# Kernel optimization log

Hardware: AMD Instinct MI355X
Metric: run time of the kernel (lower is better)

The kernel has to match this reference:

```python
import jax, jax.numpy as jnp
import numpy as np

B, L, LTXT = 4, 1024, 128
D_MODEL, TEXT_DIM = 768, 768
D_INNER, D_STATE, D_CONV, DT_RANK = 2 * D_MODEL, 16, 4, (D_MODEL + 15) // 16


def setup_inputs() -> dict:
    key = jax.random.key(0)
    ks = jax.random.split(key, 10)
    s = 0.02
    f32 = jnp.float32
    # A_log init as in mamba_ssm: A = repeat(arange(1, d_state+1))
    A_log = jnp.log(jnp.broadcast_to(jnp.arange(1, D_STATE + 1, dtype=f32), (D_INNER, D_STATE)))
    return {
        "image_tokens": jax.random.normal(ks[0], (B, L, D_MODEL), f32),
        "text_tokens": jax.random.normal(ks[1], (B, LTXT, TEXT_DIM), f32),
        "W_txt": s * jax.random.normal(ks[2], (D_MODEL, TEXT_DIM), f32),
        "b_txt": jnp.zeros((D_MODEL,), f32),
        "in_proj_w": s * jax.random.normal(ks[3], (2 * D_INNER, D_MODEL), f32),
        "conv_w": s * jax.random.normal(ks[4], (D_INNER, 1, D_CONV), f32),
        "conv_b": jnp.zeros((D_INNER,), f32),
        "x_proj_w": s * jax.random.normal(ks[5], (DT_RANK + 2 * D_STATE, D_INNER), f32),
        "dt_proj_w": s * jax.random.normal(ks[6], (D_INNER, DT_RANK), f32),
        "dt_proj_b": jnp.full((D_INNER,), -4.6, f32),  # inv-softplus of small dt init
        "A_log": A_log,
        "D": jnp.ones((D_INNER,), f32),
        "out_proj_w": s * jax.random.normal(ks[7], (D_MODEL, D_INNER), f32),
    }


def _mamba(tokens, in_proj_w, conv_w, conv_b, x_proj_w, dt_proj_w, dt_proj_b, A_log, D, out_proj_w):
    Bsz = tokens.shape[0]
    # input projection -> x, z each (B, L, d_inner)
    xz = tokens @ in_proj_w.T
    x, z = jnp.split(xz, 2, axis=-1)
    # causal depthwise conv1d over L + SiLU
    x_bdl = jnp.transpose(x, (0, 2, 1))  # (B, d_inner, L)
    x_conv = jax.lax.conv_general_dilated(
        x_bdl, conv_w, (1,), [(D_CONV - 1, 0)],
        dimension_numbers=("NCH", "OIH", "NCH"), feature_group_count=D_INNER,
    ) + conv_b[None, :, None]
    x = jax.nn.silu(jnp.transpose(x_conv, (0, 2, 1)))  # (B, L, d_inner)
    # input-dependent SSM params
    x_dbl = x @ x_proj_w.T  # (B, L, dt_rank + 2*d_state)
    dt_r = x_dbl[..., :DT_RANK]
    Bm = x_dbl[..., DT_RANK:DT_RANK + D_STATE]  # (B, L, d_state)
    Cm = x_dbl[..., DT_RANK + D_STATE:]         # (B, L, d_state)
    dt = jax.nn.softplus(dt_r @ dt_proj_w.T + dt_proj_b)  # (B, L, d_inner)
    A = -jnp.exp(A_log)  # (d_inner, d_state)

    def step(h, inp):
        dt_t, B_t, C_t, u_t = inp  # (B,d_inner),(B,d_state),(B,d_state),(B,d_inner)
        dA = jnp.exp(dt_t[:, :, None] * A)                  # (B, d_inner, d_state)
        h = dA * h + (dt_t * u_t)[:, :, None] * B_t[:, None, :]
        y = jnp.einsum("bds,bs->bd", h, C_t)
        return h, y

    h0 = jnp.zeros((Bsz, D_INNER, D_STATE), tokens.dtype)
    xs = (
        jnp.transpose(dt, (1, 0, 2)),
        jnp.transpose(Bm, (1, 0, 2)),
        jnp.transpose(Cm, (1, 0, 2)),
        jnp.transpose(x, (1, 0, 2)),
    )
    _, ys = jax.lax.scan(step, h0, xs)  # ys: (L, B, d_inner)
    y = jnp.transpose(ys, (1, 0, 2)) + x * D
    y = y * jax.nn.silu(z)
    return y @ out_proj_w.T  # (B, L, d_model)


def reference(image_tokens, text_tokens, W_txt, b_txt, in_proj_w, conv_w, conv_b,
              x_proj_w, dt_proj_w, dt_proj_b, A_log, D, out_proj_w):
    # text_pool='cls' -> take token 0
    txt = text_tokens[:, 0, :] @ W_txt.T + b_txt          # (B, d_model)
    tokens = image_tokens + txt[:, None, :]                # broadcast add
    y = _mamba(tokens, in_proj_w, conv_w, conv_b, x_proj_w,
               dt_proj_w, dt_proj_b, A_log, D, out_proj_w)
    # AdaptiveAvgPool1d(1) over sequence dim, then squeeze -> (B, d_model)
    return y.mean(axis=1)
```

## Files before the change

### kernel.cpp

```cpp
#include <hip/hip_runtime.h>
#include <math.h>

constexpr int kB   = 4;
constexpr int kL   = 1024;
constexpr int kDM  = 768;
constexpr int kDI  = 1536;
constexpr int kDS  = 16;
constexpr int kDTR = 48;
constexpr int kNX  = 80;
constexpr int kM   = kB * kL;
constexpr int kLTXT = 128;

typedef __attribute__((ext_vector_type(8))) short bf16x8;
typedef __attribute__((ext_vector_type(4))) float f32x4;

__device__ inline unsigned short f2bf(float f) {
    unsigned u = __float_as_uint(f);
    u = (u + 0x7FFFu + ((u >> 16) & 1u)) >> 16;
    return (unsigned short)u;
}

__device__ __forceinline__ void gl2lds16(const unsigned short* g, unsigned short* l) {
    __builtin_amdgcn_global_load_lds(
        (const __attribute__((address_space(1))) unsigned int*)g,
        (__attribute__((address_space(3))) unsigned int*)l, 16, 0, 0);
}

__global__ __launch_bounds__(256) void txt_kernel(
    const float* __restrict__ text, const float* __restrict__ Wt,
    const float* __restrict__ bt, float* __restrict__ txt)
{
    int gw = blockIdx.x * 4 + (threadIdx.x >> 6);
    int lane = threadIdx.x & 63;
    int b = gw / kDM;
    int j = gw - b * kDM;
    const float* trow = text + (size_t)b * kLTXT * kDM;
    const float* wrow = Wt + (size_t)j * kDM;
    float acc = 0.f;
    for (int k = lane; k < kDM; k += 64) acc = fmaf(trow[k], wrow[k], acc);
    #pragma unroll
    for (int o = 32; o; o >>= 1) acc += __shfl_xor(acc, o, 64);
    if (lane == 0) txt[gw] = acc + bt[j];
}

__global__ __launch_bounds__(256) void tokens_bf16_kernel(
    const float* __restrict__ img, const float* __restrict__ txt,
    unsigned short* __restrict__ tok)
{
    int i = blockIdx.x * 256 + threadIdx.x;
    float4 a = ((const float4*)img)[i];
    int m = i / (kDM / 4);
    int k4 = i - m * (kDM / 4);
    float4 tv = ((const float4*)(txt + (size_t)(m >> 10) * kDM))[k4];
    ushort4 o;
    o.x = f2bf(a.x + tv.x); o.y = f2bf(a.y + tv.y);
    o.z = f2bf(a.z + tv.z); o.w = f2bf(a.w + tv.w);
    ((ushort4*)tok)[i] = o;
}

__global__ __launch_bounds__(256) void castw_kernel(
    const float* __restrict__ w, unsigned short* __restrict__ o, int n4)
{
    int i = blockIdx.x * 256 + threadIdx.x;
    if (i >= n4) return;
    float4 a = ((const float4*)w)[i];
    ushort4 v;
    v.x = f2bf(a.x); v.y = f2bf(a.y); v.z = f2bf(a.z); v.w = f2bf(a.w);
    ((ushort4*)o)[i] = v;
}

__global__ __launch_bounds__(256) void mfma_inproj_kernel(
    const unsigned short* __restrict__ A, const unsigned short* __restrict__ W,
    float* __restrict__ xout, float* __restrict__ gout)
{
    __shared__ unsigned short Asm[2][128][32];
    __shared__ unsigned short Wsm[2][128][32];
    const int t = threadIdx.x;
    const int lane = t & 63;
    const int wv = t >> 6;
    const int wr = wv >> 1, wc = wv & 1;
    const int m0 = blockIdx.x * 128;
    const int n0 = blockIdx.y * 128;

    const int srow = lane >> 2;
    const int scol = (lane & 3) * 8;
    const unsigned short* agp  = A + (size_t)(m0 + wv * 32 + srow) * kDM + scol;
    const unsigned short* agp2 = agp + 16 * kDM;
    const unsigned short* wgp  = W + (size_t)(n0 + wv * 32 + srow) * kDM + scol;
    const unsigned short* wgp2 = wgp + 16 * kDM;

    auto stage = [&](int buf, int k0) {
        gl2lds16(agp  + k0, &Asm[buf][wv * 32][0]);
        gl2lds16(agp2 + k0, &Asm[buf][wv * 32 + 16][0]);
        gl2lds16(wgp  + k0, &Wsm[buf][wv * 32][0]);
        gl2lds16(wgp2 + k0, &Wsm[buf][wv * 32 + 16][0]);
    };

    f32x4 acc[4][4] = {};
    const int fr = lane & 15;
    const int fk = (lane >> 4) * 8;

    stage(0, 0);
    __syncthreads();

    int buf = 0;
    for (int k0 = 0; k0 < kDM; k0 += 32) {
        if (k0 + 32 < kDM) stage(buf ^ 1, k0 + 32);
        bf16x8 af[4], wf[4];
        #pragma unroll
        for (int i = 0; i < 4; ++i)
            af[i] = *(const bf16x8*)&Asm[buf][wr * 64 + i * 16 + fr][fk];
        #pragma unroll
        for (int j = 0; j < 4; ++j)
            wf[j] = *(const bf16x8*)&Wsm[buf][wc * 64 + j * 16 + fr][fk];
        #pragma unroll
        for (int i = 0; i < 4; ++i)
            #pragma unroll
            for (int j = 0; j < 4; ++j)
                acc[i][j] = __builtin_amdgcn_mfma_f32_16x16x32_bf16(af[i], wf[j], acc[i][j], 0, 0, 0);
        __syncthreads();
        buf ^= 1;
    }

    const int erow = (lane >> 4) * 4;
    const int ecol = lane & 15;
    #pragma unroll
    for (int i = 0; i < 4; ++i) {
        #pragma unroll
        for (int j = 0; j < 4; ++j) {
            const int gn = n0 + wc * 64 + j * 16 + ecol;
            #pragma unroll
            for (int q = 0; q < 4; ++q) {
                const int gm = m0 + wr * 64 + i * 16 + erow + q;
                float v = acc[i][j][q];
                if (gn < kDI) {
                    xout[(size_t)gm * kDI + gn] = v;
                } else {
                    gout[(size_t)gm * kDI + (gn - kDI)] = v / (1.f + __expf(-v));
                }
            }
        }
    }
}

constexpr int kKS   = 8;
constexpr int kKSEG = kDI / kKS;

__global__ __launch_bounds__(256) void xproj_splitk_kernel(
    const float* __restrict__ A, const float* __restrict__ W,
    float* __restrict__ part)
{
    __shared__ float As[16][68];
    __shared__ float Ws[16][84];
    const int t = threadIdx.x;
    const int m0 = blockIdx.x * 64;
    const int kbase = blockIdx.y * kKSEG;
    const int lrow = t >> 2, lk4 = (t & 3) << 2;
    const int ci = (t & 15) << 2;
    const int cj = (t >> 4) * 5;
    float acc[4][5] = {};
    const float* aptr = A + (size_t)(m0 + lrow) * kDI + kbase + lk4;

    for (int k0 = 0; k0 < kKSEG; k0 += 16) {
        float4 av = *(const float4*)(aptr + k0);
        if (k0) __syncthreads();
        As[lk4+0][lrow] = av.x; As[lk4+1][lrow] = av.y;
        As[lk4+2][lrow] = av.z; As[lk4+3][lrow] = av.w;
        #pragma unroll
        for (int i = 0; i < 5; ++i) {
            int idx = t + 256 * i;
            int n = idx % 80;
            int k = idx / 80;
            Ws[k][n] = W[(size_t)n * kDI + kbase + k0 + k];
        }
        __syncthreads();
        #pragma unroll
        for (int k = 0; k < 16; ++k) {
            const float4 a4 = *(const float4*)&As[k][ci];
            const float aa[4] = {a4.x, a4.y, a4.z, a4.w};
            float ww[5];
            #pragma unroll
            for (int j = 0; j < 5; ++j) ww[j] = Ws[k][cj + j];
            #pragma unroll
            for (int i = 0; i < 4; ++i)
                #pragma unroll
                for (int j = 0; j < 5; ++j)
                    acc[i][j] = fmaf(aa[i], ww[j], acc[i][j]);
        }
    }

    float* pbase = part + ((size_t)blockIdx.y * kM) * kNX;
    #pragma unroll
    for (int i = 0; i < 4; ++i)
        #pragma unroll
        for (int j = 0; j < 5; ++j)
            pbase[(size_t)(m0 + ci + i) * kNX + cj + j] = acc[i][j];
}

__global__ __launch_bounds__(256) void xproj_reduce_kernel(
    const float* __restrict__ part, float* __restrict__ xdbl)
{
    int i = blockIdx.x * 256 + threadIdx.x;
    float s = 0.f;
    #pragma unroll
    for (int k = 0; k < kKS; ++k) s += part[(size_t)k * kM * kNX + i];
    xdbl[i] = s;
}

__global__ __launch_bounds__(256) void dtproj_gemm_kernel(
    const float* __restrict__ A, const float* __restrict__ W,
    const float* __restrict__ bias, float* __restrict__ dt)
{
    __shared__ float As[16][68];
    __shared__ float Ws[16][68];
    const int t = threadIdx.x;
    const int m0 = blockIdx.x * 64;
    const int n0 = blockIdx.y * 64;
    const int lrow = t >> 2;
    const int lk4  = (t & 3) << 2;
    const int ci   = (t & 15) << 2;
    const int cj   = (t >> 4) << 2;
    float acc[4][4] = {};
    const float* aptr = A + (size_t)(m0 + lrow) * kNX + lk4;
    const float* wptr = W + (size_t)(n0 + lrow) * kDTR + lk4;

    for (int k0 = 0; k0 < kDTR; k0 += 16) {
        float4 av = *(const float4*)(aptr + k0);
        float4 wv = *(const float4*)(wptr + k0);
        if (k0) __syncthreads();
        As[lk4+0][lrow] = av.x; As[lk4+1][lrow] = av.y;
        As[lk4+2][lrow] = av.z; As[lk4+3][lrow] = av.w;
        Ws[lk4+0][lrow] = wv.x; Ws[lk4+1][lrow] = wv.y;
        Ws[lk4+2][lrow] = wv.z; Ws[lk4+3][lrow] = wv.w;
        __syncthreads();
        #pragma unroll
        for (int k = 0; k < 16; ++k) {
            const float4 a4 = *(const float4*)&As[k][ci];
            const float4 w4 = *(const float4*)&Ws[k][cj];
            const float aa[4] = {a4.x, a4.y, a4.z, a4.w};
            const float ww[4] = {w4.x, w4.y, w4.z, w4.w};
            #pragma unroll
            for (int i = 0; i < 4; ++i)
                #pragma unroll
                for (int j = 0; j < 4; ++j)
                    acc[i][j] = fmaf(aa[i], ww[j], acc[i][j]);
        }
    }

    #pragma unroll
    for (int i = 0; i < 4; ++i) {
        const int gm = m0 + ci + i;
        #pragma unroll
        for (int j = 0; j < 4; ++j) {
            const int gn = n0 + cj + j;
            float v = acc[i][j] + bias[gn];
            v = (v > 20.f) ? v : log1pf(__expf(v));
            dt[(size_t)gm * kDI + gn] = v;
        }
    }
}

__global__ __launch_bounds__(256) void conv_silu_kernel(
    const float* __restrict__ xraw, const float* __restrict__ cw,
    const float* __restrict__ cb, float* __restrict__ xout)
{
    int i = blockIdx.x * 256 + threadIdx.x;
    int d4 = i % (kDI / 4);
    int ml = i / (kDI / 4);
    int l = ml & (kL - 1);
    const int d = d4 * 4;
    float4 acc = *(const float4*)&cb[d];
    const float* base = xraw + (size_t)ml * kDI + d - 3 * (size_t)kDI;
    float4 w0 = *(const float4*)&cw[(d + 0) * 4];
    float4 w1 = *(const float4*)&cw[(d + 1) * 4];
    float4 w2 = *(const float4*)&cw[(d + 2) * 4];
    float4 w3 = *(const float4*)&cw[(d + 3) * 4];
    const float wj[4][4] = {{w0.x, w1.x, w2.x, w3.x}, {w0.y, w1.y, w2.y, w3.y},
                            {w0.z, w1.z, w2.z, w3.z}, {w0.w, w1.w, w2.w, w3.w}};
    #pragma unroll
    for (int j = 0; j < 4; ++j) {
        if (l - 3 + j >= 0) {
            float4 xv = *(const float4*)(base + (size_t)j * kDI);
            acc.x = fmaf(xv.x, wj[j][0], acc.x);
            acc.y = fmaf(xv.y, wj[j][1], acc.y);
            acc.z = fmaf(xv.z, wj[j][2], acc.z);
            acc.w = fmaf(xv.w, wj[j][3], acc.w);
        }
    }
    acc.x /= (1.f + __expf(-acc.x));
    acc.y /= (1.f + __expf(-acc.y));
    acc.z /= (1.f + __expf(-acc.z));
    acc.w /= (1.f + __expf(-acc.w));
    *(float4*)&xout[(size_t)ml * kDI + d] = acc;
}

constexpr int kNSEG = 16;
constexpr int kSEGL = kL / kNSEG;
constexpr int kCT   = 16;
constexpr int kBD   = kB * kDI;
constexpr int kP    = kBD * 16;
constexpr float kLOG2E = 1.44269504089f;

__global__ __launch_bounds__(256, 6) void scan10_kernel(
    const float* __restrict__ u, const float* __restrict__ g,
    const float* __restrict__ dt, const float* __restrict__ xdbl,
    const float* __restrict__ A_log,
    float* __restrict__ PA, float* __restrict__ QA,
    float* __restrict__ accA, float* __restrict__ wcA,
    float* __restrict__ ugA)
{
    __shared__ float uS [kCT][64];
    __shared__ float gS [kCT][64];
    __shared__ float dtS[kCT][64];
    __shared__ float bcS[kCT][34];
    const int t = threadIdx.x;
    const int blk = blockIdx.x;
    const int seg = blk & (kNSEG - 1);
    const int bd  = blk >> 4;
    const int b   = bd / 24;
    const int d0  = (bd % 24) * 64;
    const int c   = t & 63;
    const int sq  = t >> 6;
    const int d   = d0 + c;
    const int lb  = seg * kSEGL;

    f32x4 Av;
    {
        float4 al = *(const float4*)&A_log[d * kDS + sq * 4];
        Av.x = -__expf(al.x) * kLOG2E;
        Av.y = -__expf(al.y) * kLOG2E;
        Av.z = -__expf(al.z) * kLOG2E;
        Av.w = -__expf(al.w) * kLOG2E;
    }

    const float* u_base  = u  + ((size_t)b << 10) * kDI + d0;
    const float* g_base  = g  + ((size_t)b << 10) * kDI + d0;
    const float* dt_base = dt + ((size_t)b << 10) * kDI + d0;
    const float* bc_base = xdbl + ((size_t)b << 10) * kNX + kDTR;
    const int sr = t >> 4, scn = (t & 15) * 4;
    const int rb = (t & 127) >> 3, cbo = (t & 7) * 4;

    float4 ru, rg, rdt, rbc;
    auto load_chunk = [&](int l0) {
        ru  = *(const float4*)(u_base  + (size_t)(l0 + sr) * kDI + scn);
        rg  = *(const float4*)(g_base  + (size_t)(l0 + sr) * kDI + scn);
        rdt = *(const float4*)(dt_base + (size_t)(l0 + sr) * kDI + scn);
        if (t < 128) rbc = *(const float4*)(bc_base + (size_t)(l0 + rb) * kNX + cbo);
    };
    auto store_chunk = [&]() {
        *(float4*)&uS [sr][scn] = ru;
        *(float4*)&gS [sr][scn] = rg;
        *(float4*)&dtS[sr][scn] = rdt;
        if (t < 128) *(float4*)&bcS[rb][cbo] = rbc;
    };

    f32x4 h   = {0.f, 0.f, 0.f, 0.f};
    f32x4 cp  = {1.f, 1.f, 1.f, 1.f};
    f32x4 acc = {0.f, 0.f, 0.f, 0.f};
    f32x4 wc  = {0.f, 0.f, 0.f, 0.f};
    float ug = 0.f;

    load_chunk(lb);
    store_chunk();
    __syncthreads();

    #pragma unroll
    for (int ck = 0; ck < kSEGL / kCT; ++ck) {
        if (ck + 1 < kSEGL / kCT) load_chunk(lb + (ck + 1) * kCT);
        #pragma unroll 8
        for (int i = 0; i < kCT; ++i) {
            const float dtv = dtS[i][c];
            const float uv  = uS [i][c];
            const float gv  = gS [i][c];
            const f32x4 Bv = *(const f32x4*)&bcS[i][sq * 4];
            const f32x4 Cv = *(const f32x4*)&bcS[i][16 + sq * 4];
            const f32x4 pm = dtv * Av;
            f32x4 dA;
            dA.x = exp2f(pm.x); dA.y = exp2f(pm.y);
            dA.z = exp2f(pm.z); dA.w = exp2f(pm.w);
            const float dtu = dtv * uv;
            h  = dA * h + dtu * Bv;
            cp = cp * dA;
            const f32x4 cg = Cv * gv;
            acc = h * cg + acc;
            wc  = cp * cg + wc;
            ug  = fmaf(uv, gv, ug);
        }
        if (ck + 1 < kSEGL / kCT) {
            __syncthreads();
            store_chunk();
            __syncthreads();
        }
    }

    const size_t o = (size_t)seg * kP + ((size_t)sq * kBD + b * kDI + d) * 4;
    *(f32x4*)&PA[o]   = cp;
    *(f32x4*)&QA[o]   = h;
    *(f32x4*)&accA[o] = acc;
    *(f32x4*)&wcA[o]  = wc;
    if (sq == 0) ugA[(size_t)seg * kBD + b * kDI + d] = ug;
}

__global__ __launch_bounds__(256) void scan_combine_kernel(
    const float* __restrict__ PA, const float* __restrict__ QA,
    const float* __restrict__ accA, const float* __restrict__ wcA,
    const float* __restrict__ ugA, const float* __restrict__ Dvec,
    float* __restrict__ ysum)
{
    const int p = blockIdx.x * 256 + threadIdx.x;
    const int s = p & 15;
    const int bd = p >> 4;
    const size_t pbase = ((size_t)(s >> 2) * kBD + bd) * 4 + (s & 3);
    float h = 0.f, tot = 0.f;
    #pragma unroll
    for (int seg = 0; seg < kNSEG; ++seg) {
        const size_t o = (size_t)seg * kP + pbase;
        tot += accA[o] + h * wcA[o];
        h = fmaf(PA[o], h, QA[o]);
    }
    #pragma unroll
    for (int o2 = 1; o2 < 16; o2 <<= 1) tot += __shfl_xor(tot, o2, 64);
    if (s == 0) {
        float ug = 0.f;
        #pragma unroll
        for (int seg = 0; seg < kNSEG; ++seg)
            ug += ugA[(size_t)seg * kBD + bd];
        ysum[bd] = tot + Dvec[bd % kDI] * ug;
    }
}

__global__ __launch_bounds__(256) void final_kernel(
    const float* __restrict__ ysum, const float* __restrict__ Wout,
    float* __restrict__ out)
{
    int gw = blockIdx.x * 4 + (threadIdx.x >> 6);
    int lane = threadIdx.x & 63;
    int b = gw / kDM;
    int j = gw - b * kDM;
    const float* yrow = ysum + (size_t)b * kDI;
    const float* wrow = Wout + (size_t)j * kDI;
    float acc = 0.f;
    for (int k = lane; k < kDI; k += 64) acc = fmaf(yrow[k], wrow[k], acc);
    #pragma unroll
    for (int o = 32; o; o >>= 1) acc += __shfl_xor(acc, o, 64);
    if (lane == 0) out[gw] = acc * (1.f / (float)kL);
}

extern "C" void kernel_launch(void* const* d_in, const int* in_sizes, int n_in,
                              void* d_out, int out_size, void* d_ws, size_t ws_size,
                              hipStream_t stream)
{
    const float* image_tokens = (const float*)d_in[0];
    const float* text_tokens  = (const float*)d_in[1];
    const float* W_txt        = (const float*)d_in[2];
    const float* b_txt        = (const float*)d_in[3];
    const float* in_proj_w    = (const float*)d_in[4];
    const float* conv_w       = (const float*)d_in[5];
    const float* conv_b       = (const float*)d_in[6];
    const float* x_proj_w     = (const float*)d_in[7];
    const float* dt_proj_w    = (const float*)d_in[8];
    const float* dt_proj_b    = (const float*)d_in[9];
    const float* A_log        = (const float*)d_in[10];
    const float* Dvec         = (const float*)d_in[11];
    const float* out_proj_w   = (const float*)d_in[12];
    float* out = (float*)d_out;

    char* p = (char*)d_ws;
    float* txt  = (float*)p;                      p += 12288;
    float* dtreg = (float*)p;                     p += (size_t)kM * kDI * 4;
    float* xraw = (float*)p;                      p += (size_t)kM * kDI * 4;
    float* gbuf = (float*)p;                      p += (size_t)kM * kDI * 4;
    float* xbuf = (float*)p;                      p += (size_t)kM * kDI * 4;
    float* xdbl = (float*)p;                      p += (size_t)kM * kNX * 4;
    float* ysum = (float*)p;                      p += 32768;
    float* ugA  = (float*)p;                      p += (size_t)kNSEG * kBD * 4;

    unsigned short* tokb = (unsigned short*)dtreg;
    unsigned short* wb   = tokb + (size_t)kM * kDM;
    float* part = dtreg;
    float* dtb  = dtreg;
    float* PA   = xraw;
    float* QA   = PA + (size_t)kNSEG * kP;
    float* accA = QA + (size_t)kNSEG * kP;
    float* wcA  = accA + (size_t)kNSEG * kP;

    txt_kernel<<<dim3(kB * kDM / 4), dim3(256), 0, stream>>>(text_tokens, W_txt, b_txt, txt);

    tokens_bf16_kernel<<<dim3(kM * kDM / 4 / 256), dim3(256), 0, stream>>>(image_tokens, txt, tokb);

    castw_kernel<<<dim3((2 * kDI * kDM / 4 + 255) / 256), dim3(256), 0, stream>>>(
        in_proj_w, wb, 2 * kDI * kDM / 4);

    mfma_inproj_kernel<<<dim3(kM / 128, 2 * kDI / 128), dim3(256), 0, stream>>>(
        tokb, wb, xraw, gbuf);

    conv_silu_kernel<<<dim3(kM * kDI / 4 / 256), dim3(256), 0, stream>>>(
        xraw, conv_w, conv_b, xbuf);

    xproj_splitk_kernel<<<dim3(kM / 64, kKS), dim3(256), 0, stream>>>(xbuf, x_proj_w, part);
    xproj_reduce_kernel<<<dim3(kM * kNX / 256), dim3(256), 0, stream>>>(part, xdbl);

    dtproj_gemm_kernel<<<dim3(kM / 64, kDI / 64), dim3(256), 0, stream>>>(
        xdbl, dt_proj_w, dt_proj_b, dtb);

    scan10_kernel<<<dim3(kB * 24 * kNSEG), dim3(256), 0, stream>>>(
        xbuf, gbuf, dtb, xdbl, A_log, PA, QA, accA, wcA, ugA);
    scan_combine_kernel<<<dim3(kP / 256), dim3(256), 0, stream>>>(
        PA, QA, accA, wcA, ugA, Dvec, ysum);

    final_kernel<<<dim3(kB * kDM / 4), dim3(256), 0, stream>>>(ysum, out_proj_w, out);
}
```

Before: 188.3 us.

## Store gate and dt intermediates as bf16 and merge prep casts into one kernel

The silu(z) gate and softplus dt tensors are now written as bf16 instead of fp32, which halves their write traffic in the in-projection and dt-projection GEMMs and their read traffic in the scan. The scan's chunk loader is reworked so half the threads fetch 8 bf16 gate values and the other half fetch 8 bf16 dt values, widening them to fp32 in LDS. Separately, the token cast and weight cast kernels are merged into a single launch. The cost is lower precision on dt and the gate, which could move the output within tolerance.

```diff
diff --git a/kernel.cpp b/kernel.cpp
--- a/kernel.cpp
+++ b/kernel.cpp
@@ -13,11 +13,15 @@
 
 typedef __attribute__((ext_vector_type(8))) short bf16x8;
 typedef __attribute__((ext_vector_type(4))) float f32x4;
+typedef __attribute__((ext_vector_type(8))) unsigned short u16x8;
 
 __device__ inline unsigned short f2bf(float f) {
     unsigned u = __float_as_uint(f);
     u = (u + 0x7FFFu + ((u >> 16) & 1u)) >> 16;
     return (unsigned short)u;
+}
+__device__ inline float bf2f(unsigned short us) {
+    return __uint_as_float((unsigned)us << 16);
 }
 
 __device__ __forceinline__ void gl2lds16(const unsigned short* g, unsigned short* l) {
@@ -43,35 +47,34 @@
     if (lane == 0) txt[gw] = acc + bt[j];
 }
 
-__global__ __launch_bounds__(256) void tokens_bf16_kernel(
+__global__ __launch_bounds__(256) void prep_kernel(
     const float* __restrict__ img, const float* __restrict__ txt,
-    unsigned short* __restrict__ tok)
-{
-    int i = blockIdx.x * 256 + threadIdx.x;
-    float4 a = ((const float4*)img)[i];
-    int m = i / (kDM / 4);
-    int k4 = i - m * (kDM / 4);
-    float4 tv = ((const float4*)(txt + (size_t)(m >> 10) * kDM))[k4];
-    ushort4 o;
-    o.x = f2bf(a.x + tv.x); o.y = f2bf(a.y + tv.y);
-    o.z = f2bf(a.z + tv.z); o.w = f2bf(a.w + tv.w);
-    ((ushort4*)tok)[i] = o;
-}
-
-__global__ __launch_bounds__(256) void castw_kernel(
-    const float* __restrict__ w, unsigned short* __restrict__ o, int n4)
-{
-    int i = blockIdx.x * 256 + threadIdx.x;
-    if (i >= n4) return;
-    float4 a = ((const float4*)w)[i];
-    ushort4 v;
-    v.x = f2bf(a.x); v.y = f2bf(a.y); v.z = f2bf(a.z); v.w = f2bf(a.w);
-    ((ushort4*)o)[i] = v;
+    unsigned short* __restrict__ tok,
+    const float* __restrict__ w, unsigned short* __restrict__ wb)
+{
+    const int bid = blockIdx.x;
+    if (bid < 3072) {
+        int i = bid * 256 + threadIdx.x;
+        float4 a = ((const float4*)img)[i];
+        int m = i / (kDM / 4);
+        int k4 = i - m * (kDM / 4);
+        float4 tv = ((const float4*)(txt + (size_t)(m >> 10) * kDM))[k4];
+        ushort4 o;
+        o.x = f2bf(a.x + tv.x); o.y = f2bf(a.y + tv.y);
+        o.z = f2bf(a.z + tv.z); o.w = f2bf(a.w + tv.w);
+        ((ushort4*)tok)[i] = o;
+    } else {
+        int i = (bid - 3072) * 256 + threadIdx.x;
+        float4 a = ((const float4*)w)[i];
+        ushort4 v;
+        v.x = f2bf(a.x); v.y = f2bf(a.y); v.z = f2bf(a.z); v.w = f2bf(a.w);
+        ((ushort4*)wb)[i] = v;
+    }
 }
 
 __global__ __launch_bounds__(256) void mfma_inproj_kernel(
     const unsigned short* __restrict__ A, const unsigned short* __restrict__ W,
-    float* __restrict__ xout, float* __restrict__ gout)
+    float* __restrict__ xout, unsigned short* __restrict__ gout)
 {
     __shared__ unsigned short Asm[2][128][32];
     __shared__ unsigned short Wsm[2][128][32];
@@ -136,7 +139,7 @@
                 if (gn < kDI) {
                     xout[(size_t)gm * kDI + gn] = v;
                 } else {
-                    gout[(size_t)gm * kDI + (gn - kDI)] = v / (1.f + __expf(-v));
+                    gout[(size_t)gm * kDI + (gn - kDI)] = f2bf(v / (1.f + __expf(-v)));
                 }
             }
         }
@@ -209,7 +212,7 @@
 
 __global__ __launch_bounds__(256) void dtproj_gemm_kernel(
     const float* __restrict__ A, const float* __restrict__ W,
-    const float* __restrict__ bias, float* __restrict__ dt)
+    const float* __restrict__ bias, unsigned short* __restrict__ dt)
 {
     __shared__ float As[16][68];
     __shared__ float Ws[16][68];
@@ -250,13 +253,15 @@
     #pragma unroll
     for (int i = 0; i < 4; ++i) {
         const int gm = m0 + ci + i;
+        ushort4 o;
+        unsigned short* op = (unsigned short*)&o;
         #pragma unroll
         for (int j = 0; j < 4; ++j) {
-            const int gn = n0 + cj + j;
-            float v = acc[i][j] + bias[gn];
+            float v = acc[i][j] + bias[n0 + cj + j];
             v = (v > 20.f) ? v : log1pf(__expf(v));
-            dt[(size_t)gm * kDI + gn] = v;
-        }
+            op[j] = f2bf(v);
+        }
+        *(ushort4*)&dt[(size_t)gm * kDI + n0 + cj] = o;
     }
 }
 
@@ -301,9 +306,9 @@
 constexpr int kP    = kBD * 16;
 constexpr float kLOG2E = 1.44269504089f;
 
-__global__ __launch_bounds__(256, 6) void scan10_kernel(
-    const float* __restrict__ u, const float* __restrict__ g,
-    const float* __restrict__ dt, const float* __restrict__ xdbl,
+__global__ __launch_bounds__(256, 6) void scan11_kernel(
+    const float* __restrict__ u, const unsigned short* __restrict__ g,
+    const unsigned short* __restrict__ dt, const float* __restrict__ xdbl,
     const float* __restrict__ A_log,
     float* __restrict__ PA, float* __restrict__ QA,
     float* __restrict__ accA, float* __restrict__ wcA,
@@ -333,24 +338,35 @@
         Av.w = -__expf(al.w) * kLOG2E;
     }
 
-    const float* u_base  = u  + ((size_t)b << 10) * kDI + d0;
-    const float* g_base  = g  + ((size_t)b << 10) * kDI + d0;
-    const float* dt_base = dt + ((size_t)b << 10) * kDI + d0;
+    const float* u_base           = u  + ((size_t)b << 10) * kDI + d0;
+    const unsigned short* g_base  = g  + ((size_t)b << 10) * kDI + d0;
+    const unsigned short* dt_base = dt + ((size_t)b << 10) * kDI + d0;
     const float* bc_base = xdbl + ((size_t)b << 10) * kNX + kDTR;
     const int sr = t >> 4, scn = (t & 15) * 4;
-    const int rb = (t & 127) >> 3, cbo = (t & 7) * 4;
-
-    float4 ru, rg, rdt, rbc;
+    const int hr = (t & 127) >> 3, hc = ((t & 127) & 7) * 8;
+    const int rb = (t & 127) >> 3, cbo = ((t & 127) & 7) * 4;
+
+    float4 ru, rbc;
+    u16x8 rgd;
     auto load_chunk = [&](int l0) {
-        ru  = *(const float4*)(u_base  + (size_t)(l0 + sr) * kDI + scn);
-        rg  = *(const float4*)(g_base  + (size_t)(l0 + sr) * kDI + scn);
-        rdt = *(const float4*)(dt_base + (size_t)(l0 + sr) * kDI + scn);
-        if (t < 128) rbc = *(const float4*)(bc_base + (size_t)(l0 + rb) * kNX + cbo);
+        ru = *(const float4*)(u_base + (size_t)(l0 + sr) * kDI + scn);
+        if (t < 128) {
+            rgd = *(const u16x8*)(g_base + (size_t)(l0 + hr) * kDI + hc);
+            rbc = *(const float4*)(bc_base + (size_t)(l0 + rb) * kNX + cbo);
+        } else {
+            rgd = *(const u16x8*)(dt_base + (size_t)(l0 + hr) * kDI + hc);
+        }
     };
     auto store_chunk = [&]() {
-        *(float4*)&uS [sr][scn] = ru;
-        *(float4*)&gS [sr][scn] = rg;
-        *(float4*)&dtS[sr][scn] = rdt;
+        *(float4*)&uS[sr][scn] = ru;
+        float* dst = (t < 128) ? &gS[hr][hc] : &dtS[hr][hc];
+        float4 lo, hi;
+        lo.x = bf2f(rgd[0]); lo.y = bf2f(rgd[1]);
+        lo.z = bf2f(rgd[2]); lo.w = bf2f(rgd[3]);
+        hi.x = bf2f(rgd[4]); hi.y = bf2f(rgd[5]);
+        hi.z = bf2f(rgd[6]); hi.w = bf2f(rgd[7]);
+        *(float4*)(dst)     = lo;
+        *(float4*)(dst + 4) = hi;
         if (t < 128) *(float4*)&bcS[rb][cbo] = rbc;
     };
 
@@ -469,7 +485,7 @@
     float* txt  = (float*)p;                      p += 12288;
     float* dtreg = (float*)p;                     p += (size_t)kM * kDI * 4;
     float* xraw = (float*)p;                      p += (size_t)kM * kDI * 4;
-    float* gbuf = (float*)p;                      p += (size_t)kM * kDI * 4;
+    unsigned short* gbuf = (unsigned short*)p;    p += (size_t)kM * kDI * 4;
     float* xbuf = (float*)p;                      p += (size_t)kM * kDI * 4;
     float* xdbl = (float*)p;                      p += (size_t)kM * kNX * 4;
     float* ysum = (float*)p;                      p += 32768;
@@ -478,7 +494,7 @@
     unsigned short* tokb = (unsigned short*)dtreg;
     unsigned short* wb   = tokb + (size_t)kM * kDM;
     float* part = dtreg;
-    float* dtb  = dtreg;
+    unsigned short* dtb = (unsigned short*)dtreg;
     float* PA   = xraw;
     float* QA   = PA + (size_t)kNSEG * kP;
     float* accA = QA + (size_t)kNSEG * kP;
@@ -486,10 +502,8 @@
 
     txt_kernel<<<dim3(kB * kDM / 4), dim3(256), 0, stream>>>(text_tokens, W_txt, b_txt, txt);
 
-    tokens_bf16_kernel<<<dim3(kM * kDM / 4 / 256), dim3(256), 0, stream>>>(image_tokens, txt, tokb);
-
-    castw_kernel<<<dim3((2 * kDI * kDM / 4 + 255) / 256), dim3(256), 0, stream>>>(
-        in_proj_w, wb, 2 * kDI * kDM / 4);
+    prep_kernel<<<dim3(3072 + 2304), dim3(256), 0, stream>>>(
+        image_tokens, txt, tokb, in_proj_w, wb);
 
     mfma_inproj_kernel<<<dim3(kM / 128, 2 * kDI / 128), dim3(256), 0, stream>>>(
         tokb, wb, xraw, gbuf);
@@ -503,7 +517,7 @@
     dtproj_gemm_kernel<<<dim3(kM / 64, kDI / 64), dim3(256), 0, stream>>>(
         xdbl, dt_proj_w, dt_proj_b, dtb);
 
-    scan10_kernel<<<dim3(kB * 24 * kNSEG), dim3(256), 0, stream>>>(
+    scan11_kernel<<<dim3(kB * 24 * kNSEG), dim3(256), 0, stream>>>(
         xbuf, gbuf, dtb, xdbl, A_log, PA, QA, accA, wcA, ugA);
     scan_combine_kernel<<<dim3(kP / 256), dim3(256), 0, stream>>>(
         PA, QA, accA, wcA, ugA, Dvec, ysum);
```

Measured after the change: 185.5 us. About the same (-1.5%).
